# Performance work log

Measured on AMD Instinct MI355X. Metric: run time of the kernel, lower is better.

The kernel has to match this reference:

```python
import jax, jax.numpy as jnp
import numpy as np

B, N, IN_C = 8, 2048, 256
HEADS, OUT_C = 4, 128
E = 65536
BN_EPS = 1e-5


def setup_inputs() -> dict:
    key = jax.random.key(0)
    k1, k2, k3, k4 = jax.random.split(key, 4)
    x = jax.random.normal(k1, (B, N, IN_C), dtype=jnp.float32)
    edge_index = jax.random.randint(k2, (2, E), 0, N, dtype=jnp.int64)
    # Linear W: in_channels -> heads*out_channels, no bias (stored as [in, out])
    W = jax.random.normal(k3, (IN_C, HEADS * OUT_C), dtype=jnp.float32) / np.sqrt(IN_C)
    # att Linear: 2*out_channels -> 1, no bias (stored as a vector)
    a = jax.random.normal(k4, (2 * OUT_C,), dtype=jnp.float32) / np.sqrt(2 * OUT_C)
    bn_gamma = jnp.ones((OUT_C,), dtype=jnp.float32)
    bn_beta = jnp.zeros((OUT_C,), dtype=jnp.float32)
    return {"x": x, "edge_index": edge_index, "W": W, "a": a,
            "bn_gamma": bn_gamma, "bn_beta": bn_beta}


def reference(x, edge_index, W, a, bn_gamma, bn_beta):
    Bsz, Nn, _ = x.shape
    src, dst = edge_index[0], edge_index[1]
    h = (x @ W).reshape(Bsz, Nn, HEADS, OUT_C)  # [B,N,H,C]
    # att([h_src, h_dst]) == h_src @ a[:C] + h_dst @ a[C:] ; precompute per node
    s_src = jnp.einsum("bnhc,c->bnh", h, a[:OUT_C])  # [B,N,H]
    s_dst = jnp.einsum("bnhc,c->bnh", h, a[OUT_C:])
    e = s_src[:, src] + s_dst[:, dst]                 # [B,E,H]
    e = jax.nn.leaky_relu(e, negative_slope=0.2)
    e_avg = e.mean(axis=-1)                           # [B,E]
    # dense N x N attention: rows = dst, cols = src, -inf elsewhere
    attn = jnp.full((Bsz, Nn, Nn), -jnp.inf, dtype=x.dtype)
    attn = attn.at[:, dst, src].set(e_avg)
    attn = jax.nn.softmax(attn, axis=-1)
    attn = jnp.nan_to_num(attn, nan=0.0)              # rows with no edges -> 0
    # dropout is identity in eval mode
    h_flat = h.reshape(Bsz, Nn, HEADS * OUT_C)
    h_out = attn @ h_flat                             # [B,N,H*C]
    h_out = h_out.reshape(Bsz, Nn, HEADS, OUT_C).mean(axis=2)  # [B,N,C]
    # BatchNorm1d over channel dim (batch stats, biased var, affine params)
    mean = h_out.mean(axis=(0, 1))
    var = h_out.var(axis=(0, 1))
    h_out = (h_out - mean) / jnp.sqrt(var + BN_EPS) * bn_gamma + bn_beta
    return jax.nn.elu(h_out)
```

## Files before the change

kernel.cpp:

```cpp
#include <hip/hip_runtime.h>
#include <hip/hip_bf16.h>
#include <math.h>

#define BB 8
#define NN 2048
#define INC 256
#define CC 128
#define NE 65536
#define CAP 128
#define MROWS (BB*NN)
#define BN_EPS 1e-5f
#define NT 9
#define NKC 8
#define NFRAG (NT*NKC*64)
#define FPSCALE 4194304.0

typedef unsigned int uint32;
typedef unsigned long long u64;
typedef __attribute__((ext_vector_type(8))) short short8;
typedef __attribute__((ext_vector_type(4))) float f32x4;

__device__ inline ushort f2bf(float f) {
  __hip_bfloat16 b = __float2bfloat16(f);
  return reinterpret_cast<ushort&>(b);
}
__device__ inline float bf2f(ushort h) {
  return __uint_as_float(((uint32)h) << 16);
}

__device__ inline void load_edge(const void* ei, int is64, int e, int& s, int& d) {
  if (is64) {
    const long long* p = (const long long*)ei;
    s = (int)p[e]; d = (int)p[NE + e];
  } else {
    const int* p = (const int*)ei;
    s = p[e]; d = p[NE + e];
  }
}

__global__ __launch_bounds__(256) void k_prep(const float* __restrict__ W,
                                              const float* __restrict__ a,
                                              const int* __restrict__ ei32,
                                              uint4* __restrict__ pack,
                                              int* __restrict__ flag,
                                              int* __restrict__ row_cnt,
                                              u64* __restrict__ bins) {
  __shared__ float Wl[8][520];
  __shared__ float Wms[8][132];
  __shared__ float Was[8][8];
  __shared__ float av[256];
  int m = blockIdx.x, tid = threadIdx.x;
  if (m < 8) row_cnt[m * 256 + tid] = 0;
  if (m == 8) {
    #pragma unroll
    for (int i = 0; i < 8; ++i) bins[tid * 8 + i] = 0ull;
  }
  if (m == 0 && tid == 0) {
    int nz = 0;
    for (int t = 1; t < 128; t += 2) nz |= (ei32[t] != 0);
    *flag = nz ? 0 : 1;
  }
  av[tid] = a[tid];
  const float4* Wg = (const float4*)(W + (size_t)m * 8 * 512);
  #pragma unroll
  for (int i = 0; i < 4; ++i) {
    int idx = tid + i * 256;
    int r = idx >> 7, c4 = idx & 127;
    *(float4*)&Wl[r][c4 * 4] = Wg[idx];
  }
  __syncthreads();
  {
    int c = tid & 127, half = tid >> 7;
    #pragma unroll
    for (int ii = 0; ii < 4; ++ii) {
      int r = half * 4 + ii;
      Wms[r][c] = 0.25f * (Wl[r][c] + Wl[r][128 + c] + Wl[r][256 + c] + Wl[r][384 + c]);
    }
  }
  {
    int i8 = tid >> 5, c2 = tid & 31;
    float p[8];
    #pragma unroll
    for (int j = 0; j < 8; ++j) p[j] = 0.0f;
    #pragma unroll
    for (int t4 = 0; t4 < 4; ++t4) {
      int cc = c2 + t4 * 32;
      float asrc = av[cc], adst = av[128 + cc];
      #pragma unroll
      for (int h = 0; h < 4; ++h) {
        float w = Wl[i8][h * 128 + cc];
        p[h] += w * asrc;
        p[4 + h] += w * adst;
      }
    }
    #pragma unroll
    for (int off = 16; off > 0; off >>= 1)
      #pragma unroll
      for (int j = 0; j < 8; ++j) p[j] += __shfl_xor(p[j], off, 64);
    if (c2 < 8) Was[i8][c2] = p[c2];
  }
  __syncthreads();
  if (tid < 144) {
    int t = tid >> 4, l16 = tid & 15;
    int cch = t * 16 + l16;
    int kc = m >> 2, g = m & 3;
    uint32 h[8];
    #pragma unroll
    for (int j = 0; j < 8; ++j) {
      float v = 0.0f;
      if (cch < CC) v = Wms[j][cch];
      else if (cch < CC + 8) v = Was[j][cch - CC];
      h[j] = (uint32)f2bf(v);
    }
    uint4 u;
    u.x = h[0] | (h[1] << 16);
    u.y = h[2] | (h[3] << 16);
    u.z = h[4] | (h[5] << 16);
    u.w = h[6] | (h[7] << 16);
    pack[(t * NKC + kc) * 64 + g * 16 + l16] = u;
  }
}

__global__ __launch_bounds__(512) void k_gemm(const float* __restrict__ x,
                                              const uint4* __restrict__ pack,
                                              const void* __restrict__ ei,
                                              const int* __restrict__ flag,
                                              ushort* __restrict__ hm,
                                              float* __restrict__ s,
                                              int* __restrict__ row_cnt,
                                              int* __restrict__ row_src) {
  __shared__ uint4 lp[NFRAG];
  int tid = threadIdx.x;
  if (tid < 256) {
    int e = blockIdx.x * 256 + tid;
    int is64 = *flag;
    int src, dst;
    load_edge(ei, is64, e, src, dst);
    int pos = atomicAdd(&row_cnt[dst], 1);
    if (pos < CAP) row_src[dst * CAP + pos] = src;
  }
  #pragma unroll
  for (int i = 0; i < 9; ++i) lp[i * 512 + tid] = pack[i * 512 + tid];

  int lane = tid & 63, wv = tid >> 6;
  int rt = wv & 3, th = wv >> 2;
  int g = lane >> 4;
  int xrow = blockIdx.x * 64 + rt * 16 + (lane & 15);
  const float* xr = x + (size_t)xrow * INC;

  short8 xf[8];
  #pragma unroll
  for (int kc = 0; kc < 8; ++kc) {
    f32x4 xa = *(const f32x4*)(xr + kc * 32 + g * 8);
    f32x4 xb = *(const f32x4*)(xr + kc * 32 + g * 8 + 4);
    short8 t;
    t[0] = (short)f2bf(xa[0]); t[1] = (short)f2bf(xa[1]);
    t[2] = (short)f2bf(xa[2]); t[3] = (short)f2bf(xa[3]);
    t[4] = (short)f2bf(xb[0]); t[5] = (short)f2bf(xb[1]);
    t[6] = (short)f2bf(xb[2]); t[7] = (short)f2bf(xb[3]);
    xf[kc] = t;
  }
  __syncthreads();

  f32x4 acc[4];
  f32x4 accE = (f32x4)(0.0f);
  #pragma unroll
  for (int i = 0; i < 4; ++i) acc[i] = (f32x4)(0.0f);

  const short8* fr = (const short8*)lp;
  int tb = th * 4;
  #pragma unroll
  for (int kc = 0; kc < NKC; ++kc) {
    #pragma unroll
    for (int i = 0; i < 4; ++i) {
      short8 af = fr[((tb + i) * NKC + kc) * 64 + lane];
      acc[i] = __builtin_amdgcn_mfma_f32_16x16x32_bf16(af, xf[kc], acc[i], 0, 0, 0);
    }
    short8 ae = fr[(8 * NKC + kc) * 64 + lane];
    accE = __builtin_amdgcn_mfma_f32_16x16x32_bf16(ae, xf[kc], accE, 0, 0, 0);
  }

  ushort* hrow = hm + (size_t)xrow * CC;
  #pragma unroll
  for (int i = 0; i < 4; ++i) {
    int t = tb + i;
    uint32 p0 = (uint32)f2bf(acc[i][0]) | ((uint32)f2bf(acc[i][1]) << 16);
    uint32 p1 = (uint32)f2bf(acc[i][2]) | ((uint32)f2bf(acc[i][3]) << 16);
    *(uint2*)(hrow + t * 16 + g * 4) = make_uint2(p0, p1);
  }
  if (th == 1 && g < 2) {
    *(f32x4*)(s + (size_t)xrow * 8 + g * 4) = accE;
  }
}

__device__ inline float edge_e(f32x4 ss, f32x4 sd) {
  float sum = 0.0f;
  #pragma unroll
  for (int h = 0; h < 4; ++h) {
    float v = ss[h] + sd[h];
    sum += (v > 0.0f) ? v : 0.2f * v;
  }
  return 0.25f * sum;
}

__global__ __launch_bounds__(256) void k_agg(const int* __restrict__ row_cnt,
                                             const int* __restrict__ row_src,
                                             const float* __restrict__ s,
                                             const uint32* __restrict__ hm32,
                                             uint32* __restrict__ hout,
                                             u64* __restrict__ bins) {
  __shared__ int rsrc[CAP], csrc[CAP];
  __shared__ float swgt[8][CAP];
  __shared__ f32x4 red[256];
  __shared__ int wcnt[2];
  int d = blockIdx.x, tid = threadIdx.x;
  int lane = tid & 63, wv = tid >> 6;
  int k0 = row_cnt[d]; if (k0 > CAP) k0 = CAP;

  if (tid < k0) rsrc[tid] = row_src[d * CAP + tid];
  __syncthreads();
  int keep = 0;
  if (tid < k0) {
    keep = 1;
    int sv = rsrc[tid];
    for (int q = 0; q < tid; ++q) if (rsrc[q] == sv) { keep = 0; break; }
  }
  u64 mask = __ballot(keep);
  int pos = __popcll(mask & ((1ull << lane) - 1ull));
  if (lane == 0 && wv < 2) wcnt[wv] = (int)__popcll(mask);
  __syncthreads();
  int base = (wv == 1) ? wcnt[0] : 0;
  if (keep) csrc[base + pos] = rsrc[tid];
  __syncthreads();
  int kd = wcnt[0] + wcnt[1];
  if (tid < kd) {
    int sv = csrc[tid], r = 0;
    for (int q = 0; q < kd; ++q) r += (csrc[q] < sv) ? 1 : 0;
    rsrc[r] = sv;
  }
  __syncthreads();

  int b0 = wv, b1 = wv + 4;
  const float* sb0 = s + (size_t)b0 * NN * 8;
  const float* sb1 = s + (size_t)b1 * NN * 8;
  f32x4 sd0 = *(const f32x4*)(sb0 + (size_t)d * 8 + 4);
  f32x4 sd1 = *(const f32x4*)(sb1 + (size_t)d * 8 + 4);
  float v00 = -INFINITY, v01 = -INFINITY, v10 = -INFINITY, v11 = -INFINITY;
  if (lane < kd) {
    int r = rsrc[lane];
    f32x4 s0 = *(const f32x4*)(sb0 + (size_t)r * 8);
    f32x4 s1 = *(const f32x4*)(sb1 + (size_t)r * 8);
    v00 = edge_e(s0, sd0);
    v10 = edge_e(s1, sd1);
  }
  if (lane + 64 < kd) {
    int r = rsrc[lane + 64];
    f32x4 s0 = *(const f32x4*)(sb0 + (size_t)r * 8);
    f32x4 s1 = *(const f32x4*)(sb1 + (size_t)r * 8);
    v01 = edge_e(s0, sd0);
    v11 = edge_e(s1, sd1);
  }
  float m0 = fmaxf(v00, v01), m1 = fmaxf(v10, v11);
  #pragma unroll
  for (int off = 32; off > 0; off >>= 1) {
    m0 = fmaxf(m0, __shfl_xor(m0, off, 64));
    m1 = fmaxf(m1, __shfl_xor(m1, off, 64));
  }
  float e00 = (lane < kd)      ? expf(v00 - m0) : 0.0f;
  float e01 = (lane + 64 < kd) ? expf(v01 - m0) : 0.0f;
  float e10 = (lane < kd)      ? expf(v10 - m1) : 0.0f;
  float e11 = (lane + 64 < kd) ? expf(v11 - m1) : 0.0f;
  float sum0 = e00 + e01, sum1 = e10 + e11;
  #pragma unroll
  for (int off = 32; off > 0; off >>= 1) {
    sum0 += __shfl_xor(sum0, off, 64);
    sum1 += __shfl_xor(sum1, off, 64);
  }
  float inv0 = (kd > 0) ? 1.0f / sum0 : 0.0f;
  float inv1 = (kd > 0) ? 1.0f / sum1 : 0.0f;
  swgt[wv][lane]      = e00 * inv0;
  swgt[wv][lane + 64] = e01 * inv0;
  swgt[b1][lane]      = e10 * inv1;
  swgt[b1][lane + 64] = e11 * inv1;

  float a0 = 0.0f, a1 = 0.0f, a2 = 0.0f, a3 = 0.0f;
  const uint32* hb0 = hm32 + (size_t)b0 * NN * (CC / 2);
  const uint32* hb1 = hm32 + (size_t)b1 * NN * (CC / 2);
  #pragma unroll 4
  for (int j = 0; j < kd; ++j) {
    int r = rsrc[j];
    float w0 = swgt[wv][j], w1 = swgt[b1][j];
    uint32 u0 = hb0[(size_t)r * (CC / 2) + lane];
    uint32 u1 = hb1[(size_t)r * (CC / 2) + lane];
    a0 += w0 * bf2f((ushort)(u0 & 0xffffu));
    a1 += w0 * bf2f((ushort)(u0 >> 16));
    a2 += w1 * bf2f((ushort)(u1 & 0xffffu));
    a3 += w1 * bf2f((ushort)(u1 >> 16));
  }
  hout[((size_t)b0 * NN + d) * (CC / 2) + lane] =
      (uint32)f2bf(a0) | ((uint32)f2bf(a1) << 16);
  hout[((size_t)b1 * NN + d) * (CC / 2) + lane] =
      (uint32)f2bf(a2) | ((uint32)f2bf(a3) << 16);

  f32x4 r4;
  r4[0] = a0 + a2; r4[1] = a0 * a0 + a2 * a2;
  r4[2] = a1 + a3; r4[3] = a1 * a1 + a3 * a3;
  red[tid] = r4;
  __syncthreads();
  if (wv == 0) {
    f32x4 t = red[lane] + red[lane + 64] + red[lane + 128] + red[lane + 192];
    u64* bb = bins + (size_t)(d & 7) * (CC * 2);
    atomicAdd(&bb[4 * lane + 0], (u64)(long long)llrint((double)t[0] * FPSCALE));
    atomicAdd(&bb[4 * lane + 1], (u64)(long long)llrint((double)t[1] * FPSCALE));
    atomicAdd(&bb[4 * lane + 2], (u64)(long long)llrint((double)t[2] * FPSCALE));
    atomicAdd(&bb[4 * lane + 3], (u64)(long long)llrint((double)t[3] * FPSCALE));
  }
}

__global__ __launch_bounds__(256) void k_elu(const uint32* __restrict__ hout,
                                             const u64* __restrict__ bins,
                                             const float* __restrict__ gamma,
                                             const float* __restrict__ beta,
                                             float* __restrict__ out) {
  __shared__ float bsc[CC], bsh[CC];
  int tid = threadIdx.x;
  if (tid < CC) {
    long long S = 0, Q = 0;
    #pragma unroll
    for (int bin = 0; bin < 8; ++bin) {
      S += (long long)bins[bin * (CC * 2) + 2 * tid];
      Q += (long long)bins[bin * (CC * 2) + 2 * tid + 1];
    }
    double mean = (double)S / FPSCALE / (double)MROWS;
    double var  = (double)Q / FPSCALE / (double)MROWS - mean * mean;
    if (var < 0.0) var = 0.0;
    float scale = gamma[tid] / sqrtf((float)var + BN_EPS);
    bsc[tid] = scale;
    bsh[tid] = beta[tid] - (float)mean * scale;
  }
  __syncthreads();
  int pbase = blockIdx.x * 1024 + tid;
  #pragma unroll
  for (int i = 0; i < 4; ++i) {
    int p = pbase + i * 256;
    int cp = p & 63;
    uint32 u = hout[p];
    float y0 = bf2f((ushort)(u & 0xffffu)) * bsc[2 * cp]     + bsh[2 * cp];
    float y1 = bf2f((ushort)(u >> 16))     * bsc[2 * cp + 1] + bsh[2 * cp + 1];
    float2 o;
    o.x = (y0 > 0.0f) ? y0 : expm1f(y0);
    o.y = (y1 > 0.0f) ? y1 : expm1f(y1);
    *(float2*)(out + 2 * (size_t)p) = o;
  }
}

extern "C" void kernel_launch(void* const* d_in, const int* in_sizes, int n_in,
                              void* d_out, int out_size, void* d_ws, size_t ws_size,
                              hipStream_t stream) {
  const float* x     = (const float*)d_in[0];
  const void*  ei    = d_in[1];
  const float* W     = (const float*)d_in[2];
  const float* a     = (const float*)d_in[3];
  const float* gamma = (const float*)d_in[4];
  const float* beta  = (const float*)d_in[5];
  float* out = (float*)d_out;

  char* p = (char*)d_ws;
  ushort* hm   = (ushort*)p; p += (size_t)MROWS * CC * 2;
  uint32* hout = (uint32*)p; p += (size_t)MROWS * CC * 2;
  float* s    = (float*)p; p += (size_t)MROWS * 8 * 4;
  uint4* pack = (uint4*)p; p += (size_t)NFRAG * 16;
  u64* bins   = (u64*)p;   p += 8 * CC * 2 * 8;
  int* flag   = (int*)p;   p += 256;
  int* row_cnt  = (int*)p; p += NN * 4;
  int* row_src  = (int*)p; p += (size_t)NN * CAP * 4;

  k_prep<<<32, 256, 0, stream>>>(W, a, (const int*)ei, pack, flag, row_cnt, bins);
  k_gemm<<<MROWS / 64, 512, 0, stream>>>(x, pack, ei, flag, hm, s, row_cnt, row_src);
  k_agg<<<NN, 256, 0, stream>>>(row_cnt, row_src, s, (const uint32*)hm, hout, bins);
  k_elu<<<(MROWS * CC / 2) / 1024, 256, 0, stream>>>(hout, bins, gamma, beta, out);
}
```

Baseline: 65.27 us.

## Interleave batch dimension in node features so gathers fetch contiguous rows

The GEMM now writes h and the attention scores in node-major, batch-interleaved layout ([N][B][C]). Each gathered source node's features for all 8 batches then form one contiguous 2KB block, which the aggregation kernel reads with one uint2 per thread, replacing two strided 256B row reads. The batch-norm partial reduction is restructured to match the new thread-to-channel mapping, adding an extra barrier and more shared memory for the split sum and square buffers.

```diff
diff --git a/kernel.cpp b/kernel.cpp
--- a/kernel.cpp
+++ b/kernel.cpp
@@ -36,6 +36,16 @@
     const int* p = (const int*)ei;
     s = p[e]; d = p[NE + e];
   }
+}
+
+__device__ inline float edge_e(f32x4 ss, f32x4 sd) {
+  float sum = 0.0f;
+  #pragma unroll
+  for (int h = 0; h < 4; ++h) {
+    float v = ss[h] + sd[h];
+    sum += (v > 0.0f) ? v : 0.2f * v;
+  }
+  return 0.25f * sum;
 }
 
 __global__ __launch_bounds__(256) void k_prep(const float* __restrict__ W,
@@ -146,6 +156,7 @@
   int rt = wv & 3, th = wv >> 2;
   int g = lane >> 4;
   int xrow = blockIdx.x * 64 + rt * 16 + (lane & 15);
+  int b = xrow >> 11, n = xrow & (NN - 1);
   const float* xr = x + (size_t)xrow * INC;
 
   short8 xf[8];
@@ -180,7 +191,7 @@
     accE = __builtin_amdgcn_mfma_f32_16x16x32_bf16(ae, xf[kc], accE, 0, 0, 0);
   }
 
-  ushort* hrow = hm + (size_t)xrow * CC;
+  ushort* hrow = hm + ((size_t)n * BB + b) * CC;
   #pragma unroll
   for (int i = 0; i < 4; ++i) {
     int t = tb + i;
@@ -189,29 +200,20 @@
     *(uint2*)(hrow + t * 16 + g * 4) = make_uint2(p0, p1);
   }
   if (th == 1 && g < 2) {
-    *(f32x4*)(s + (size_t)xrow * 8 + g * 4) = accE;
-  }
-}
-
-__device__ inline float edge_e(f32x4 ss, f32x4 sd) {
-  float sum = 0.0f;
-  #pragma unroll
-  for (int h = 0; h < 4; ++h) {
-    float v = ss[h] + sd[h];
-    sum += (v > 0.0f) ? v : 0.2f * v;
-  }
-  return 0.25f * sum;
+    *(f32x4*)(s + ((size_t)n * BB + b) * 8 + g * 4) = accE;
+  }
 }
 
 __global__ __launch_bounds__(256) void k_agg(const int* __restrict__ row_cnt,
                                              const int* __restrict__ row_src,
                                              const float* __restrict__ s,
-                                             const uint32* __restrict__ hm32,
-                                             uint32* __restrict__ hout,
+                                             const uint2* __restrict__ hm2,
+                                             uint2* __restrict__ hout2,
                                              u64* __restrict__ bins) {
   __shared__ int rsrc[CAP], csrc[CAP];
   __shared__ float swgt[8][CAP];
-  __shared__ f32x4 red[256];
+  __shared__ f32x4 redS[256];
+  __shared__ f32x4 redQ[256];
   __shared__ int wcnt[2];
   int d = blockIdx.x, tid = threadIdx.x;
   int lane = tid & 63, wv = tid >> 6;
@@ -240,80 +242,84 @@
   }
   __syncthreads();
 
-  int b0 = wv, b1 = wv + 4;
-  const float* sb0 = s + (size_t)b0 * NN * 8;
-  const float* sb1 = s + (size_t)b1 * NN * 8;
-  f32x4 sd0 = *(const f32x4*)(sb0 + (size_t)d * 8 + 4);
-  f32x4 sd1 = *(const f32x4*)(sb1 + (size_t)d * 8 + 4);
-  float v00 = -INFINITY, v01 = -INFINITY, v10 = -INFINITY, v11 = -INFINITY;
-  if (lane < kd) {
-    int r = rsrc[lane];
-    f32x4 s0 = *(const f32x4*)(sb0 + (size_t)r * 8);
-    f32x4 s1 = *(const f32x4*)(sb1 + (size_t)r * 8);
-    v00 = edge_e(s0, sd0);
-    v10 = edge_e(s1, sd1);
-  }
-  if (lane + 64 < kd) {
-    int r = rsrc[lane + 64];
-    f32x4 s0 = *(const f32x4*)(sb0 + (size_t)r * 8);
-    f32x4 s1 = *(const f32x4*)(sb1 + (size_t)r * 8);
-    v01 = edge_e(s0, sd0);
-    v11 = edge_e(s1, sd1);
-  }
-  float m0 = fmaxf(v00, v01), m1 = fmaxf(v10, v11);
-  #pragma unroll
-  for (int off = 32; off > 0; off >>= 1) {
-    m0 = fmaxf(m0, __shfl_xor(m0, off, 64));
-    m1 = fmaxf(m1, __shfl_xor(m1, off, 64));
-  }
-  float e00 = (lane < kd)      ? expf(v00 - m0) : 0.0f;
-  float e01 = (lane + 64 < kd) ? expf(v01 - m0) : 0.0f;
-  float e10 = (lane < kd)      ? expf(v10 - m1) : 0.0f;
-  float e11 = (lane + 64 < kd) ? expf(v11 - m1) : 0.0f;
-  float sum0 = e00 + e01, sum1 = e10 + e11;
-  #pragma unroll
-  for (int off = 32; off > 0; off >>= 1) {
-    sum0 += __shfl_xor(sum0, off, 64);
-    sum1 += __shfl_xor(sum1, off, 64);
-  }
-  float inv0 = (kd > 0) ? 1.0f / sum0 : 0.0f;
-  float inv1 = (kd > 0) ? 1.0f / sum1 : 0.0f;
-  swgt[wv][lane]      = e00 * inv0;
-  swgt[wv][lane + 64] = e01 * inv0;
-  swgt[b1][lane]      = e10 * inv1;
-  swgt[b1][lane + 64] = e11 * inv1;
-
-  float a0 = 0.0f, a1 = 0.0f, a2 = 0.0f, a3 = 0.0f;
-  const uint32* hb0 = hm32 + (size_t)b0 * NN * (CC / 2);
-  const uint32* hb1 = hm32 + (size_t)b1 * NN * (CC / 2);
+  {
+    int b0 = wv, b1 = wv + 4;
+    f32x4 sd0 = *(const f32x4*)(s + ((size_t)d * BB + b0) * 8 + 4);
+    f32x4 sd1 = *(const f32x4*)(s + ((size_t)d * BB + b1) * 8 + 4);
+    float v00 = -INFINITY, v01 = -INFINITY, v10 = -INFINITY, v11 = -INFINITY;
+    if (lane < kd) {
+      int r = rsrc[lane];
+      f32x4 s0 = *(const f32x4*)(s + ((size_t)r * BB + b0) * 8);
+      f32x4 s1 = *(const f32x4*)(s + ((size_t)r * BB + b1) * 8);
+      v00 = edge_e(s0, sd0);
+      v10 = edge_e(s1, sd1);
+    }
+    if (lane + 64 < kd) {
+      int r = rsrc[lane + 64];
+      f32x4 s0 = *(const f32x4*)(s + ((size_t)r * BB + b0) * 8);
+      f32x4 s1 = *(const f32x4*)(s + ((size_t)r * BB + b1) * 8);
+      v01 = edge_e(s0, sd0);
+      v11 = edge_e(s1, sd1);
+    }
+    float m0 = fmaxf(v00, v01), m1 = fmaxf(v10, v11);
+    #pragma unroll
+    for (int off = 32; off > 0; off >>= 1) {
+      m0 = fmaxf(m0, __shfl_xor(m0, off, 64));
+      m1 = fmaxf(m1, __shfl_xor(m1, off, 64));
+    }
+    float e00 = (lane < kd)      ? expf(v00 - m0) : 0.0f;
+    float e01 = (lane + 64 < kd) ? expf(v01 - m0) : 0.0f;
+    float e10 = (lane < kd)      ? expf(v10 - m1) : 0.0f;
+    float e11 = (lane + 64 < kd) ? expf(v11 - m1) : 0.0f;
+    float sum0 = e00 + e01, sum1 = e10 + e11;
+    #pragma unroll
+    for (int off = 32; off > 0; off >>= 1) {
+      sum0 += __shfl_xor(sum0, off, 64);
+      sum1 += __shfl_xor(sum1, off, 64);
+    }
+    float inv0 = (kd > 0) ? 1.0f / sum0 : 0.0f;
+    float inv1 = (kd > 0) ? 1.0f / sum1 : 0.0f;
+    swgt[b0][lane]      = e00 * inv0;
+    swgt[b0][lane + 64] = e01 * inv0;
+    swgt[b1][lane]      = e10 * inv1;
+    swgt[b1][lane + 64] = e11 * inv1;
+  }
+  __syncthreads();
+
+  int b = tid >> 5;
+  int q32 = tid & 31;
+  float ac0 = 0, ac1 = 0, ac2 = 0, ac3 = 0;
   #pragma unroll 4
   for (int j = 0; j < kd; ++j) {
     int r = rsrc[j];
-    float w0 = swgt[wv][j], w1 = swgt[b1][j];
-    uint32 u0 = hb0[(size_t)r * (CC / 2) + lane];
-    uint32 u1 = hb1[(size_t)r * (CC / 2) + lane];
-    a0 += w0 * bf2f((ushort)(u0 & 0xffffu));
-    a1 += w0 * bf2f((ushort)(u0 >> 16));
-    a2 += w1 * bf2f((ushort)(u1 & 0xffffu));
-    a3 += w1 * bf2f((ushort)(u1 >> 16));
-  }
-  hout[((size_t)b0 * NN + d) * (CC / 2) + lane] =
-      (uint32)f2bf(a0) | ((uint32)f2bf(a1) << 16);
-  hout[((size_t)b1 * NN + d) * (CC / 2) + lane] =
-      (uint32)f2bf(a2) | ((uint32)f2bf(a3) << 16);
-
-  f32x4 r4;
-  r4[0] = a0 + a2; r4[1] = a0 * a0 + a2 * a2;
-  r4[2] = a1 + a3; r4[3] = a1 * a1 + a3 * a3;
-  red[tid] = r4;
-  __syncthreads();
-  if (wv == 0) {
-    f32x4 t = red[lane] + red[lane + 64] + red[lane + 128] + red[lane + 192];
+    float w = swgt[b][j];
+    uint2 u = hm2[(size_t)r * 256 + tid];
+    ac0 += w * bf2f((ushort)(u.x & 0xffffu));
+    ac1 += w * bf2f((ushort)(u.x >> 16));
+    ac2 += w * bf2f((ushort)(u.y & 0xffffu));
+    ac3 += w * bf2f((ushort)(u.y >> 16));
+  }
+  uint2 o;
+  o.x = (uint32)f2bf(ac0) | ((uint32)f2bf(ac1) << 16);
+  o.y = (uint32)f2bf(ac2) | ((uint32)f2bf(ac3) << 16);
+  hout2[((size_t)b * NN + d) * 32 + q32] = o;
+
+  f32x4 rs, rq;
+  rs[0] = ac0; rs[1] = ac1; rs[2] = ac2; rs[3] = ac3;
+  rq[0] = ac0 * ac0; rq[1] = ac1 * ac1; rq[2] = ac2 * ac2; rq[3] = ac3 * ac3;
+  redS[tid] = rs; redQ[tid] = rq;
+  __syncthreads();
+  if (tid < 32) {
+    f32x4 ts = redS[tid], tq = redQ[tid];
+    #pragma unroll
+    for (int k = 1; k < 8; ++k) { ts += redS[tid + 32 * k]; tq += redQ[tid + 32 * k]; }
     u64* bb = bins + (size_t)(d & 7) * (CC * 2);
-    atomicAdd(&bb[4 * lane + 0], (u64)(long long)llrint((double)t[0] * FPSCALE));
-    atomicAdd(&bb[4 * lane + 1], (u64)(long long)llrint((double)t[1] * FPSCALE));
-    atomicAdd(&bb[4 * lane + 2], (u64)(long long)llrint((double)t[2] * FPSCALE));
-    atomicAdd(&bb[4 * lane + 3], (u64)(long long)llrint((double)t[3] * FPSCALE));
+    int cb = tid * 4;
+    #pragma unroll
+    for (int i = 0; i < 4; ++i) {
+      atomicAdd(&bb[2 * (cb + i) + 0], (u64)(long long)llrint((double)ts[i] * FPSCALE));
+      atomicAdd(&bb[2 * (cb + i) + 1], (u64)(long long)llrint((double)tq[i] * FPSCALE));
+    }
   }
 }
 
@@ -377,6 +383,7 @@
 
   k_prep<<<32, 256, 0, stream>>>(W, a, (const int*)ei, pack, flag, row_cnt, bins);
   k_gemm<<<MROWS / 64, 512, 0, stream>>>(x, pack, ei, flag, hm, s, row_cnt, row_src);
-  k_agg<<<NN, 256, 0, stream>>>(row_cnt, row_src, s, (const uint32*)hm, hout, bins);
+  k_agg<<<NN, 256, 0, stream>>>(row_cnt, row_src, s, (const uint2*)hm,
+                                (uint2*)hout, bins);
   k_elu<<<(MROWS * CC / 2) / 1024, 256, 0, stream>>>(hout, bins, gamma, beta, out);
 }
```

New measurement: 88.56 us. 35.7% more time.
